# Performance work log

Hardware: AMD Instinct MI355X
Metric: run time of the kernel (lower is better)

The kernel has to match this reference:

```python
import jax, jax.numpy as jnp
import numpy as np

N, E, G = 50000, 800000, 128
IN, HID, HEAD = 1280, 256, 4
DH = HID // HEAD
EPS = 1e-5
ATT_SCALE = 1.0 / np.sqrt(1280.0).astype(np.float32)  # hardcoded in source


def _seg_softmax(x, seg, n):
    # softmax over segments along axis 0; x: [K] or [K, H]
    m = jax.ops.segment_max(x, seg, num_segments=n)
    e = jnp.exp(x - m[seg])
    s = jax.ops.segment_sum(e, seg, num_segments=n)
    return e / s[seg]


def _bn(x, g, b):
    # eval-mode BatchNorm1d with init running stats (mean=0, var=1)
    return g * x * (1.0 / np.sqrt(1.0 + EPS)) + b


def _ln(x, g, b):
    mu = x.mean(-1, keepdims=True)
    var = ((x - mu) ** 2).mean(-1, keepdims=True)
    return g * (x - mu) / jnp.sqrt(var + EPS) + b


def setup_inputs() -> dict:
    key = jax.random.key(0)
    ks = jax.random.split(key, 40)
    rn = lambda i, shp, s=0.05: jax.random.normal(ks[i], shp, jnp.float32) * s
    inp = {
        "h": jax.random.normal(ks[0], (N, IN), jnp.float32),
        "gcn_w0": rn(1, (IN, HID)), "gcn_b0": rn(2, (HID,), 0.01),
        "gcn_w1": rn(3, (HID, HID)), "gcn_b1": rn(4, (HID,), 0.01),
        "bn_gcn0_g": 1.0 + rn(5, (HID,), 0.1), "bn_gcn0_b": rn(6, (HID,), 0.01),
        "bn_gcn1_g": 1.0 + rn(7, (HID,), 0.1), "bn_gcn1_b": rn(8, (HID,), 0.01),
        "gat_w0": rn(9, (IN, HID)), "gat_al0": rn(10, (HEAD, DH)), "gat_ar0": rn(11, (HEAD, DH)), "gat_bias0": rn(12, (HID,), 0.01),
        "gat_w1": rn(13, (HID, HID)), "gat_al1": rn(14, (HEAD, DH)), "gat_ar1": rn(15, (HEAD, DH)), "gat_bias1": rn(16, (HID,), 0.01),
        "bn_gat0_g": 1.0 + rn(17, (HID,), 0.1), "bn_gat0_b": rn(18, (HID,), 0.01),
        "bn_gat1_g": 1.0 + rn(19, (HID,), 0.1), "bn_gat1_b": rn(20, (HID,), 0.01),
        "gate_w": rn(21, (2 * HID, HID)), "gate_b": rn(22, (HID,), 0.01),
        "qw": rn(23, (HEAD, HID, HID)), "kw": rn(24, (HEAD, HID, HID)), "vw": rn(25, (HEAD, HID, HID)),
        "ct_w": rn(26, (HEAD * HID, HID)),
        "ff_w1": rn(27, (HID, 2 * HID)), "ff_b1": rn(28, (2 * HID,), 0.01),
        "ff_w2": rn(29, (2 * HID, HID)), "ff_b2": rn(30, (HID,), 0.01),
        "ln_g": 1.0 + rn(31, (HID,), 0.1), "ln_b": rn(32, (HID,), 0.01),
        "src": jax.random.randint(ks[33], (E,), 0, N, jnp.int32),
        "dst": jax.random.randint(ks[34], (E,), 0, N, jnp.int32),
        "gid": jnp.sort(jax.random.randint(ks[35], (N,), 0, G, jnp.int32)),
        "num_graphs": G,
    }
    return inp


def reference(h, gcn_w0, gcn_b0, gcn_w1, gcn_b1, bn_gcn0_g, bn_gcn0_b, bn_gcn1_g, bn_gcn1_b,
              gat_w0, gat_al0, gat_ar0, gat_bias0, gat_w1, gat_al1, gat_ar1, gat_bias1,
              bn_gat0_g, bn_gat0_b, bn_gat1_g, bn_gat1_b, gate_w, gate_b,
              qw, kw, vw, ct_w, ff_w1, ff_b1, ff_w2, ff_b2, ln_g, ln_b,
              src, dst, gid, num_graphs):
    n = h.shape[0]
    ones_e = jnp.ones(src.shape[0], h.dtype)
    # dgl.mean_nodes per graph
    cnt = jnp.clip(jax.ops.segment_sum(jnp.ones(n, h.dtype), gid, num_segments=num_graphs), 1.0)
    init_avg_h = jax.ops.segment_sum(h, gid, num_segments=num_graphs) / cnt[:, None]
    # GraphConv norm='both', degrees clamped to >=1
    deg_out = jnp.clip(jax.ops.segment_sum(ones_e, src, num_segments=n), 1.0)
    deg_in = jnp.clip(jax.ops.segment_sum(ones_e, dst, num_segments=n), 1.0)
    ns, nd = deg_out ** -0.5, deg_in ** -0.5

    def gcn(x, w, b):
        m = (x * ns[:, None]) @ w  # [N, HID]
        return jax.ops.segment_sum(m[src], dst, num_segments=n) * nd[:, None] + b

    hg = jax.nn.relu(_bn(gcn(h, gcn_w0, gcn_b0), bn_gcn0_g, bn_gcn0_b))
    hg = jax.nn.relu(_bn(gcn(hg, gcn_w1, gcn_b1), bn_gcn1_g, bn_gcn1_b)) + hg

    def gat(x, w, al, ar, b):
        f = (x @ w).reshape(n, HEAD, DH)
        el = (f * al).sum(-1)  # [N, HEAD]
        er = (f * ar).sum(-1)
        e = jax.nn.leaky_relu(el[src] + er[dst], 0.2)  # [E, HEAD]
        alpha = _seg_softmax(e, dst, n)  # edge softmax over incoming edges
        out = jax.ops.segment_sum(alpha[:, :, None] * f[src], dst, num_segments=n)
        return out.reshape(n, HID) + b

    ha = jax.nn.elu(_bn(gat(h, gat_w0, gat_al0, gat_ar0, gat_bias0), bn_gat0_g, bn_gat0_b))
    ha = jax.nn.elu(_bn(gat(ha, gat_w1, gat_al1, gat_ar1, gat_bias1), bn_gat1_g, bn_gat1_b)) + ha

    gate = jax.nn.sigmoid(jnp.concatenate([hg, ha], axis=1) @ gate_w + gate_b)
    x = gate * hg + (1.0 - gate) * ha  # residue_h

    # transformer_block: per-graph node softmax attention
    q = jnp.einsum('nd,hde->nhe', x, qw)
    k = jnp.einsum('nd,hde->nhe', x, kw)
    v = jnp.einsum('nd,hde->nhe', x, vw)
    att = (q * k).sum(-1) * ATT_SCALE  # [N, HEAD]
    alpha = _seg_softmax(att, gid, num_graphs)  # dgl.softmax_nodes per head
    mo = (v * alpha[:, :, None]).reshape(n, HEAD * HID) @ ct_w
    x1 = _ln(mo + x, ln_g, ln_b)
    x2 = _ln(jax.nn.relu(x1 @ ff_w1 + ff_b1) @ ff_w2 + ff_b2 + x1, ln_g, ln_b)

    readout = jax.ops.segment_sum(x2, gid, num_segments=num_graphs)
    return readout, init_avg_h
```

## Files before the change

### kernel.cpp

```cpp
#include <hip/hip_runtime.h>

#define NN 50000
#define NE 800000
#define NG 128
#define DIN 1280
#define HIDDEN 256
#define BNS 0.9999950000374997f
#define ATT_SCALE 0.027950849718747373f
#define LN_EPS 1e-5f

typedef __attribute__((ext_vector_type(8))) short short8;
typedef __attribute__((ext_vector_type(4))) float floatx4;

__device__ __forceinline__ float b2f(unsigned short u) {
  return __uint_as_float(((unsigned int)u) << 16);
}
__device__ __forceinline__ unsigned short f2b(float f) {
  unsigned int x = __float_as_uint(f);
  x += 0x7fffu + ((x >> 16) & 1u);
  return (unsigned short)(x >> 16);
}

__global__ void transpose_w_k(const float* __restrict__ src, unsigned short* __restrict__ dst,
                              int K, int Nc) {
// ... 20 lines not shown
}

__global__ void v_transpose_k(const float* __restrict__ vw, unsigned short* __restrict__ dst) {
  int idx = blockIdx.x * 256 + threadIdx.x;
  if (idx >= 1024 * 256) return;
  int r = idx >> 8;
  int d = idx & 255;
  int hh = r >> 8;
  int e2 = r & 255;
  dst[(size_t)(1024 + r) * 256 + d] = f2b(vw[((size_t)hh * 256 + d) * 256 + e2]);
}

__global__ void cvt_avg_k(const float* __restrict__ h, const int* __restrict__ gid,
                          unsigned short* __restrict__ h_bf, float* __restrict__ out1) {
  int row0 = blockIdx.x * 50;
  int tid = threadIdx.x;
  float acc[5] = {0, 0, 0, 0, 0};
  int cur_g = gid[row0];
  for (int r = 0; r < 50; ++r) {
    int row = row0 + r;
    int g = gid[row];
    if (g != cur_g) {
#pragma unroll
      for (int j = 0; j < 5; ++j) {
        atomicAdd(&out1[(size_t)cur_g * DIN + j * 256 + tid], acc[j]);
        acc[j] = 0.f;
      }
      cur_g = g;
    }
#pragma unroll
    for (int j = 0; j < 5; ++j) {
      float v = h[(size_t)row * DIN + j * 256 + tid];
      acc[j] += v;
      h_bf[(size_t)row * DIN + j * 256 + tid] = f2b(v);
    }
  }
#pragma unroll
  for (int j = 0; j < 5; ++j)
    atomicAdd(&out1[(size_t)cur_g * DIN + j * 256 + tid], acc[j]);
}

__global__ void div_avg_k(const int* __restrict__ start, float* __restrict__ out1) {
  int idx = blockIdx.x * 256 + threadIdx.x;
  if (idx >= NG * DIN) return;
  int g = idx / DIN;
  float cnt = (float)(start[g + 1] - start[g]);
  if (cnt < 1.f) cnt = 1.f;
  out1[idx] /= cnt;
}

__global__ void graph_bounds_k(const int* __restrict__ gid, int* __restrict__ start, int n) {
  int i = blockIdx.x * 256 + threadIdx.x;
  if (i >= n) return;
  int g = gid[i];
  if (i == 0) {
    for (int gg = 0; gg <= g; ++gg) start[gg] = 0;
  } else {
    int gp = gid[i - 1];
    for (int gg = gp + 1; gg <= g; ++gg) start[gg] = i;
  }
  if (i == n - 1) {
    for (int gg = g + 1; gg <= NG; ++gg) start[gg] = n;
  }
}

__global__ void degrees_k(const int* __restrict__ src, const int* __restrict__ dst,
                          int* __restrict__ deg_out, int* __restrict__ deg_in, int e) {
  int i = blockIdx.x * 256 + threadIdx.x;
  if (i >= e) return;
  atomicAdd(&deg_out[src[i]], 1);
  atomicAdd(&deg_in[dst[i]], 1);
}

__global__ void invsqrt_k(const int* __restrict__ deg_out, const int* __restrict__ deg_in,
                          float* __restrict__ ns, float* __restrict__ nd, int n) {
  int i = blockIdx.x * 256 + threadIdx.x;
  if (i >= n) return;
  int a = deg_out[i]; if (a < 1) a = 1;
  int b = deg_in[i];  if (b < 1) b = 1;
  ns[i] = rsqrtf((float)a);
  nd[i] = rsqrtf((float)b);
}

__global__ void scan_k(const int* __restrict__ deg, int* __restrict__ row_ptr, int n) {
  __shared__ int buf[1024];
  __shared__ int carry_s;
  int tid = threadIdx.x;
  if (tid == 0) carry_s = 0;
  __syncthreads();
  for (int base = 0; base < n; base += 1024) {
    int i = base + tid;
    int v = (i < n) ? deg[i] : 0;
    buf[tid] = v;
    __syncthreads();
    for (int off = 1; off < 1024; off <<= 1) {
      int t = (tid >= off) ? buf[tid - off] : 0;
      __syncthreads();
      buf[tid] += t;
      __syncthreads();
    }
    int carry = carry_s;
    if (i < n) row_ptr[i] = carry + buf[tid] - v;
    __syncthreads();
    if (tid == 1023) carry_s = carry + buf[1023];
    __syncthreads();
  }
  if (tid == 0) row_ptr[n] = carry_s;
}

__global__ void fill_csr_k(const int* __restrict__ src, const int* __restrict__ dst,
                           const int* __restrict__ row_ptr, int* __restrict__ fill,
                           int* __restrict__ csr_src, int e) {
  int i = blockIdx.x * 256 + threadIdx.x;
  if (i >= e) return;
  int d = dst[i];
  int pos = row_ptr[d] + atomicAdd(&fill[d], 1);
  csr_src[pos] = src[i];
}

template <int MODE>
__global__ __launch_bounds__(256, 2) void gemm_bf16(const unsigned short* __restrict__ A,
                                                    const unsigned short* __restrict__ Bt,
                                                    void* __restrict__ Cout,
                                                    const float* __restrict__ bias,
                                                    int M, int K, int Nc) {
  __shared__ unsigned short lA[8192];
  __shared__ unsigned short lB[8192];
  const int tid = threadIdx.x;
  const int m0 = blockIdx.x * 128;
  const int n0 = blockIdx.y * 128;
  const int w = tid >> 6;
  const int lane = tid & 63;
  const int wr = (w >> 1) * 64;
  const int wc = (w & 1) * 64;
  const int quad = lane >> 4;
  const int l15 = lane & 15;
  const int js = tid & 7;
  const int mbase = tid >> 3;

  floatx4 acc[4][4];
#pragma unroll
  for (int i = 0; i < 4; ++i)
#pragma unroll
    for (int j = 0; j < 4; ++j) acc[i][j] = (floatx4)0.0f;

  for (int k0 = 0; k0 < K; k0 += 64) {
    __syncthreads();
#pragma unroll
    for (int it = 0; it < 4; ++it) {
      int m = it * 32 + mbase;
      int gm = m0 + m;
      if (gm >= M) gm = M - 1;
      uint4 va = *(const uint4*)(A + (size_t)gm * K + k0 + js * 8);
      int ci_ = js * 128 + (m ^ js);
      *(uint4*)(lA + ci_ * 8) = va;
      int gn = n0 + m;
      uint4 vb = *(const uint4*)(Bt + (size_t)gn * K + k0 + js * 8);
      *(uint4*)(lB + ci_ * 8) = vb;
    }
    __syncthreads();
#pragma unroll
    for (int ks = 0; ks < 2; ++ks) {
      int kb = ks * 4 + quad;
      short8 af[4], bfr[4];
#pragma unroll
      for (int ri = 0; ri < 4; ++ri) {
        int r = wr + ri * 16 + l15;
        af[ri] = *(const short8*)(lA + (kb * 128 + (r ^ kb)) * 8);
      }
#pragma unroll
      for (int ci = 0; ci < 4; ++ci) {
        int c = wc + ci * 16 + l15;
        bfr[ci] = *(const short8*)(lB + (kb * 128 + (c ^ kb)) * 8);
      }
#pragma unroll
      for (int ri = 0; ri < 4; ++ri)
#pragma unroll
        for (int ci = 0; ci < 4; ++ci)
          acc[ri][ci] = __builtin_amdgcn_mfma_f32_16x16x32_bf16(af[ri], bfr[ci], acc[ri][ci], 0, 0, 0);
    }
  }
#pragma unroll
  for (int ri = 0; ri < 4; ++ri) {
    int row = m0 + wr + ri * 16 + quad * 4;
#pragma unroll
    for (int ci = 0; ci < 4; ++ci) {
      int col = n0 + wc + ci * 16 + l15;
      float bv = (MODE == 2) ? bias[col] : 0.f;
#pragma unroll
      for (int r = 0; r < 4; ++r) {
        if (row + r < M) {
          float v = acc[ri][ci][r];
          if (MODE == 2) { v += bv; v = fmaxf(v, 0.f); }
          if (MODE == 1)
            ((float*)Cout)[(size_t)(row + r) * Nc + col] = v;
          else
            ((unsigned short*)Cout)[(size_t)(row + r) * Nc + col] = f2b(v);
        }
      }
    }
  }
}

__global__ void gcn_agg_k(const unsigned short* __restrict__ m, int ldm,
                          const int* __restrict__ row_ptr, const int* __restrict__ csr_src,
                          const float* __restrict__ ns, const float* __restrict__ nd,
                          const float* __restrict__ bias,
                          const float* __restrict__ bng, const float* __restrict__ bnb,
                          const unsigned short* __restrict__ resid, int ldr,
                          unsigned short* __restrict__ out, int ldo) {
  int node = blockIdx.x * 4 + (threadIdx.x >> 6);
  if (node >= NN) return;
  int lane = threadIdx.x & 63;
  int s = row_ptr[node], e = row_ptr[node + 1];
  float a0 = 0, a1 = 0, a2 = 0, a3 = 0;
  for (int i = s; i < e; ++i) {
    int u = csr_src[i];
    float w = ns[u];
    ushort4 v = *(const ushort4*)(m + (size_t)u * ldm + lane * 4);
    a0 += w * b2f(v.x); a1 += w * b2f(v.y); a2 += w * b2f(v.z); a3 += w * b2f(v.w);
  }
  float ndv = nd[node];
  int col = lane * 4;
  float vals[4] = {a0, a1, a2, a3};
  ushort4 o;
#pragma unroll
  for (int c = 0; c < 4; ++c) {
    float v = vals[c] * ndv + bias[col + c];
    v = bng[col + c] * v * BNS + bnb[col + c];
    v = fmaxf(v, 0.f);
    if (resid) v += b2f(resid[(size_t)node * ldr + col + c]);
    ((unsigned short*)&o)[c] = f2b(v);
  }
  *(ushort4*)(out + (size_t)node * ldo + col) = o;
}

__global__ void elr_k(const unsigned short* __restrict__ f, int ldf,
                      const float* __restrict__ al, const float* __restrict__ ar,
                      float* __restrict__ elr) {
  int node = blockIdx.x * 4 + (threadIdx.x >> 6);
  if (node >= NN) return;
  int lane = threadIdx.x & 63;
  int head = lane >> 4;
  int col = lane * 4;
  int dcol = col & 63;
  ushort4 v = *(const ushort4*)(f + (size_t)node * ldf + col);
  float pl = 0, pr = 0;
#pragma unroll
  for (int c = 0; c < 4; ++c) {
    float x = b2f(((unsigned short*)&v)[c]);
    pl += x * al[head * 64 + dcol + c];
    pr += x * ar[head * 64 + dcol + c];
  }
#pragma unroll
  for (int off = 1; off < 16; off <<= 1) {
    pl += __shfl_xor(pl, off);
    pr += __shfl_xor(pr, off);
  }
  if ((lane & 15) == 0) {
    elr[(size_t)node * 8 + head] = pl;
    elr[(size_t)node * 8 + 4 + head] = pr;
  }
}

__global__ void gat_agg_k(const unsigned short* __restrict__ f, int ldf,
                          const int* __restrict__ row_ptr, const int* __restrict__ csr_src,
                          const float* __restrict__ elr,
                          const float* __restrict__ bias,
                          const float* __restrict__ bng, const float* __restrict__ bnb,
                          const unsigned short* __restrict__ resid, int ldr,
                          unsigned short* __restrict__ out, int ldo) {
  int node = blockIdx.x * 4 + (threadIdx.x >> 6);
  if (node >= NN) return;
  int lane = threadIdx.x & 63;
  int s = row_ptr[node], e = row_ptr[node + 1];
  float4 er = *(const float4*)(elr + (size_t)node * 8 + 4);
  float m0 = -1e30f, m1 = -1e30f, m2 = -1e30f, m3 = -1e30f;
  for (int i = s + lane; i < e; i += 64) {
    int u = csr_src[i];
    float4 el = *(const float4*)(elr + (size_t)u * 8);
    float t;
    t = el.x + er.x; t = t > 0.f ? t : 0.2f * t; m0 = fmaxf(m0, t);
    t = el.y + er.y; t = t > 0.f ? t : 0.2f * t; m1 = fmaxf(m1, t);
    t = el.z + er.z; t = t > 0.f ? t : 0.2f * t; m2 = fmaxf(m2, t);
    t = el.w + er.w; t = t > 0.f ? t : 0.2f * t; m3 = fmaxf(m3, t);
  }
#pragma unroll
  for (int off = 1; off < 64; off <<= 1) {
    m0 = fmaxf(m0, __shfl_xor(m0, off));
    m1 = fmaxf(m1, __shfl_xor(m1, off));
    m2 = fmaxf(m2, __shfl_xor(m2, off));
    m3 = fmaxf(m3, __shfl_xor(m3, off));
  }
  float s0 = 0, s1 = 0, s2 = 0, s3 = 0;
  for (int i = s + lane; i < e; i += 64) {
    int u = csr_src[i];
    float4 el = *(const float4*)(elr + (size_t)u * 8);
    float t;
    t = el.x + er.x; t = t > 0.f ? t : 0.2f * t; s0 += expf(t - m0);
    t = el.y + er.y; t = t > 0.f ? t : 0.2f * t; s1 += expf(t - m1);
    t = el.z + er.z; t = t > 0.f ? t : 0.2f * t; s2 += expf(t - m2);
    t = el.w + er.w; t = t > 0.f ? t : 0.2f * t; s3 += expf(t - m3);
  }
#pragma unroll
  for (int off = 1; off < 64; off <<= 1) {
    s0 += __shfl_xor(s0, off);
    s1 += __shfl_xor(s1, off);
    s2 += __shfl_xor(s2, off);
    s3 += __shfl_xor(s3, off);
  }
  int head = lane >> 4;
  float erh = head == 0 ? er.x : head == 1 ? er.y : head == 2 ? er.z : er.w;
  float mh = head == 0 ? m0 : head == 1 ? m1 : head == 2 ? m2 : m3;
  float sh = head == 0 ? s0 : head == 1 ? s1 : head == 2 ? s2 : s3;
  float inv_sh = (sh > 0.f) ? 1.f / sh : 0.f;
  float a0 = 0, a1 = 0, a2 = 0, a3 = 0;
  for (int i = s; i < e; ++i) {
    int u = csr_src[i];
    float t = elr[(size_t)u * 8 + head] + erh;
    t = t > 0.f ? t : 0.2f * t;
    float wgt = expf(t - mh) * inv_sh;
    ushort4 v = *(const ushort4*)(f + (size_t)u * ldf + lane * 4);
    a0 += wgt * b2f(v.x); a1 += wgt * b2f(v.y); a2 += wgt * b2f(v.z); a3 += wgt * b2f(v.w);
  }
  int col = lane * 4;
  float vals[4] = {a0, a1, a2, a3};
  ushort4 o;
#pragma unroll
  for (int c = 0; c < 4; ++c) {
    float v = vals[c] + bias[col + c];
    v = bng[col + c] * v * BNS + bnb[col + c];
    v = (v > 0.f) ? v : (expf(v) - 1.f);
    if (resid) v += b2f(resid[(size_t)node * ldr + col + c]);
    ((unsigned short*)&o)[c] = f2b(v);
  }
  *(ushort4*)(out + (size_t)node * ldo + col) = o;
}

__global__ void combine_k(const float* __restrict__ glogit, const float* __restrict__ gate_b,
                          const unsigned short* __restrict__ xcat,
                          float* __restrict__ xf, unsigned short* __restrict__ xb) {
  int idx = blockIdx.x * 256 + threadIdx.x;
  if (idx >= NN * 64) return;
  int node = idx >> 6;
  int c = (idx & 63) * 4;
  float4 gl = *(const float4*)(glogit + (size_t)node * HIDDEN + c);
  ushort4 hgv = *(const ushort4*)(xcat + (size_t)node * 512 + c);
  ushort4 hav = *(const ushort4*)(xcat + (size_t)node * 512 + 256 + c);
  float4 o;
  float g;
  g = 1.f / (1.f + expf(-(gl.x + gate_b[c + 0]))); o.x = g * b2f(hgv.x) + (1.f - g) * b2f(hav.x);
  g = 1.f / (1.f + expf(-(gl.y + gate_b[c + 1]))); o.y = g * b2f(hgv.y) + (1.f - g) * b2f(hav.y);
  g = 1.f / (1.f + expf(-(gl.z + gate_b[c + 2]))); o.z = g * b2f(hgv.z) + (1.f - g) * b2f(hav.z);
  g = 1.f / (1.f + expf(-(gl.w + gate_b[c + 3]))); o.w = g * b2f(hgv.w) + (1.f - g) * b2f(hav.w);
  *(float4*)(xf + (size_t)node * HIDDEN + c) = o;
  ushort4 ob;
  ob.x = f2b(o.x); ob.y = f2b(o.y); ob.z = f2b(o.z); ob.w = f2b(o.w);
  *(ushort4*)(xb + (size_t)node * HIDDEN + c) = ob;
}

__global__ void att2_k(const unsigned short* __restrict__ yv, const unsigned short* __restrict__ xb,
                       float* __restrict__ att) {
  int node = blockIdx.x * 4 + (threadIdx.x >> 6);
  if (node >= NN) return;
  int lane = threadIdx.x & 63;
  const unsigned short* y = yv + (size_t)node * 2048;
  ushort4 xv = *(const ushort4*)(xb + (size_t)node * 256 + lane * 4);
  float x0 = b2f(xv.x), x1 = b2f(xv.y), x2 = b2f(xv.z), x3 = b2f(xv.w);
#pragma unroll
  for (int h = 0; h < 4; ++h) {
    ushort4 yv4 = *(const ushort4*)(y + h * 256 + lane * 4);
    float p = b2f(yv4.x) * x0 + b2f(yv4.y) * x1 + b2f(yv4.z) * x2 + b2f(yv4.w) * x3;
#pragma unroll
    for (int off = 1; off < 64; off <<= 1) p += __shfl_xor(p, off);
    if (lane == 0) att[(size_t)node * 4 + h] = p * ATT_SCALE;
  }
}

__global__ void gsoftmax_k(const float* __restrict__ att, const int* __restrict__ start,
                           float* __restrict__ alpha) {
  int g = blockIdx.x;
  int s = start[g], e = start[g + 1];
  int tid = threadIdx.x;
  __shared__ float red[256];
  __shared__ float mh[4], sh[4];
  float lm[4] = {-1e30f, -1e30f, -1e30f, -1e30f};
  for (int i = s + tid; i < e; i += 256) {
    float4 a = *(const float4*)(att + (size_t)i * 4);
    lm[0] = fmaxf(lm[0], a.x); lm[1] = fmaxf(lm[1], a.y);
    lm[2] = fmaxf(lm[2], a.z); lm[3] = fmaxf(lm[3], a.w);
  }
#pragma unroll
  for (int h = 0; h < 4; ++h) {
    red[tid] = lm[h]; __syncthreads();
    for (int off = 128; off > 0; off >>= 1) {
      if (tid < off) red[tid] = fmaxf(red[tid], red[tid + off]);
      __syncthreads();
    }
    if (tid == 0) mh[h] = red[0];
    __syncthreads();
  }
  float ls[4] = {0, 0, 0, 0};
  for (int i = s + tid; i < e; i += 256) {
    float4 a = *(const float4*)(att + (size_t)i * 4);
    ls[0] += expf(a.x - mh[0]); ls[1] += expf(a.y - mh[1]);
    ls[2] += expf(a.z - mh[2]); ls[3] += expf(a.w - mh[3]);
  }
#pragma unroll
  for (int h = 0; h < 4; ++h) {
    red[tid] = ls[h]; __syncthreads();
    for (int off = 128; off > 0; off >>= 1) {
      if (tid < off) red[tid] += red[tid + off];
      __syncthreads();
    }
    if (tid == 0) sh[h] = red[0];
    __syncthreads();
  }
  for (int i = s + tid; i < e; i += 256) {
    float4 a = *(const float4*)(att + (size_t)i * 4);
    float4 o;
    o.x = expf(a.x - mh[0]) / sh[0];
    o.y = expf(a.y - mh[1]) / sh[1];
    o.z = expf(a.z - mh[2]) / sh[2];
    o.w = expf(a.w - mh[3]) / sh[3];
    *(float4*)(alpha + (size_t)i * 4) = o;
  }
}

__global__ void scalev_k(const unsigned short* __restrict__ yv, const float* __restrict__ alpha,
                         unsigned short* __restrict__ vs) {
  int idx = blockIdx.x * 256 + threadIdx.x;
  if (idx >= NN * 256) return;
  int node = idx >> 8;
  int c = (idx & 255) * 4;
  int h = c >> 8;
  float a = alpha[(size_t)node * 4 + h];
  ushort4 v = *(const ushort4*)(yv + (size_t)node * 2048 + 1024 + c);
  ushort4 o;
  o.x = f2b(b2f(v.x) * a); o.y = f2b(b2f(v.y) * a);
  o.z = f2b(b2f(v.z) * a); o.w = f2b(b2f(v.w) * a);
  *(ushort4*)(vs + (size_t)node * 1024 + c) = o;
}

__global__ void ln1_k(const float* __restrict__ mo, const float* __restrict__ x,
                      const float* __restrict__ g, const float* __restrict__ b,
                      float* __restrict__ x1f, unsigned short* __restrict__ x1b) {
  int node = blockIdx.x * 4 + (threadIdx.x >> 6);
  if (node >= NN) return;
  int lane = threadIdx.x & 63;
  int c = lane * 4;
  float4 a = *(const float4*)(mo + (size_t)node * HIDDEN + c);
  float4 xx = *(const float4*)(x + (size_t)node * HIDDEN + c);
  float v0 = a.x + xx.x, v1 = a.y + xx.y, v2 = a.z + xx.z, v3 = a.w + xx.w;
  float sm = v0 + v1 + v2 + v3;
#pragma unroll
  for (int off = 1; off < 64; off <<= 1) sm += __shfl_xor(sm, off);
  float mu = sm * (1.f / 256.f);
  float d0 = v0 - mu, d1 = v1 - mu, d2 = v2 - mu, d3 = v3 - mu;
  float sq = d0 * d0 + d1 * d1 + d2 * d2 + d3 * d3;
#pragma unroll
  for (int off = 1; off < 64; off <<= 1) sq += __shfl_xor(sq, off);
  float inv = rsqrtf(sq * (1.f / 256.f) + LN_EPS);
  float4 o;
  o.x = g[c + 0] * d0 * inv + b[c + 0];
  o.y = g[c + 1] * d1 * inv + b[c + 1];
  o.z = g[c + 2] * d2 * inv + b[c + 2];
  o.w = g[c + 3] * d3 * inv + b[c + 3];
  *(float4*)(x1f + (size_t)node * HIDDEN + c) = o;
  ushort4 ob;
  ob.x = f2b(o.x); ob.y = f2b(o.y); ob.z = f2b(o.z); ob.w = f2b(o.w);
  *(ushort4*)(x1b + (size_t)node * HIDDEN + c) = ob;
}

__global__ void ln2_k(const float* __restrict__ ff2o, const float* __restrict__ ffb2,
                      const float* __restrict__ x1f,
                      const float* __restrict__ g, const float* __restrict__ b,
                      float* __restrict__ x2) {
  int node = blockIdx.x * 4 + (threadIdx.x >> 6);
  if (node >= NN) return;
  int lane = threadIdx.x & 63;
  int c = lane * 4;
  float4 a = *(const float4*)(ff2o + (size_t)node * HIDDEN + c);
  float4 xx = *(const float4*)(x1f + (size_t)node * HIDDEN + c);
  float v0 = a.x + ffb2[c + 0] + xx.x, v1 = a.y + ffb2[c + 1] + xx.y;
  float v2 = a.z + ffb2[c + 2] + xx.z, v3 = a.w + ffb2[c + 3] + xx.w;
  float sm = v0 + v1 + v2 + v3;
#pragma unroll
  for (int off = 1; off < 64; off <<= 1) sm += __shfl_xor(sm, off);
  float mu = sm * (1.f / 256.f);
  float d0 = v0 - mu, d1 = v1 - mu, d2 = v2 - mu, d3 = v3 - mu;
  float sq = d0 * d0 + d1 * d1 + d2 * d2 + d3 * d3;
#pragma unroll
  for (int off = 1; off < 64; off <<= 1) sq += __shfl_xor(sq, off);
  float inv = rsqrtf(sq * (1.f / 256.f) + LN_EPS);
  float4 o;
  o.x = g[c + 0] * d0 * inv + b[c + 0];
  o.y = g[c + 1] * d1 * inv + b[c + 1];
  o.z = g[c + 2] * d2 * inv + b[c + 2];
  o.w = g[c + 3] * d3 * inv + b[c + 3];
  *(float4*)(x2 + (size_t)node * HIDDEN + c) = o;
}

__global__ void readout_k(const float* __restrict__ x2, const int* __restrict__ start,
                          float* __restrict__ out0) {
  int g = blockIdx.x;
  int c = threadIdx.x;
  float acc = 0.f;
  for (int i = start[g]; i < start[g + 1]; ++i) acc += x2[(size_t)i * HIDDEN + c];
  out0[(size_t)g * HIDDEN + c] = acc;
}

static const size_t OFF_BUFA   = 0;
static const size_t OFF_XCAT   = 307200000;
static const size_t OFF_GLOGIT = OFF_XCAT + 51200000;
static const size_t OFF_XF     = OFF_GLOGIT + 51200000;
static const size_t OFF_XB     = OFF_XF + 51200000;
static const size_t OFF_VS     = OFF_XB + 25600000;
static const size_t OFF_ATT    = OFF_VS + 102400000;
static const size_t OFF_ALPHA  = OFF_ATT + 800000;
static const size_t OFF_ELR0   = OFF_ALPHA + 800000;
static const size_t OFF_ELR1   = OFF_ELR0 + 1600000;
static const size_t OFF_START  = OFF_ELR1 + 1600000;
static const size_t OFF_DEGO   = OFF_START + 1024;
static const size_t OFF_DEGI   = OFF_DEGO + 200704;
static const size_t OFF_NS     = OFF_DEGI + 200704;
static const size_t OFF_ND     = OFF_NS + 200704;
static const size_t OFF_ROWP   = OFF_ND + 200704;
static const size_t OFF_FILL   = OFF_ROWP + 200704;
static const size_t OFF_CSRS   = OFF_FILL + 200704;
static const size_t OFF_W01T   = OFF_CSRS + 3200000;
static const size_t OFF_W1T    = OFF_W01T + 1310720;
static const size_t OFF_W1GT   = OFF_W1T + 131072;
static const size_t OFF_GATEWT = OFF_W1GT + 131072;
static const size_t OFF_WMVT   = OFF_GATEWT + 262144;
static const size_t OFF_CTWT   = OFF_WMVT + 1572864;
static const size_t OFF_FFW1T  = OFF_CTWT + 524288;
static const size_t OFF_FFW2T  = OFF_FFW1T + 262144;
static const size_t WS_NEED    = OFF_FFW2T + 262144;

extern "C" void kernel_launch(void* const* d_in, const int* in_sizes, int n_in,
                              void* d_out, int out_size, void* d_ws, size_t ws_size,
                              hipStream_t stream) {
  if (ws_size < WS_NEED) return;

  const float* h       = (const float*)d_in[0];
  const float* gcn_w0  = (const float*)d_in[1];
  const float* gcn_b0  = (const float*)d_in[2];
  const float* gcn_w1  = (const float*)d_in[3];
  const float* gcn_b1  = (const float*)d_in[4];
  const float* bn_gcn0_g = (const float*)d_in[5];
  const float* bn_gcn0_b = (const float*)d_in[6];
  const float* bn_gcn1_g = (const float*)d_in[7];
  const float* bn_gcn1_b = (const float*)d_in[8];
  const float* gat_w0  = (const float*)d_in[9];
  const float* gat_al0 = (const float*)d_in[10];
  const float* gat_ar0 = (const float*)d_in[11];
  const float* gat_bias0 = (const float*)d_in[12];
  const float* gat_w1  = (const float*)d_in[13];
  const float* gat_al1 = (const float*)d_in[14];
  const float* gat_ar1 = (const float*)d_in[15];
  const float* gat_bias1 = (const float*)d_in[16];
  const float* bn_gat0_g = (const float*)d_in[17];
  const float* bn_gat0_b = (const float*)d_in[18];
  const float* bn_gat1_g = (const float*)d_in[19];
  const float* bn_gat1_b = (const float*)d_in[20];
  const float* gate_w  = (const float*)d_in[21];
  const float* gate_b  = (const float*)d_in[22];
  const float* qw      = (const float*)d_in[23];
  const float* kw      = (const float*)d_in[24];
  const float* vw      = (const float*)d_in[25];
  const float* ct_w    = (const float*)d_in[26];
  const float* ff_w1   = (const float*)d_in[27];
  const float* ff_b1   = (const float*)d_in[28];
  const float* ff_w2   = (const float*)d_in[29];
  const float* ff_b2   = (const float*)d_in[30];
  const float* ln_g    = (const float*)d_in[31];
  const float* ln_b    = (const float*)d_in[32];
  const int* srcv = (const int*)d_in[33];
  const int* dstv = (const int*)d_in[34];
  const int* gid  = (const int*)d_in[35];

  char* ws = (char*)d_ws;
  unsigned short* h_bf = (unsigned short*)(ws + OFF_BUFA);
  unsigned short* c01  = (unsigned short*)(ws + OFF_BUFA + 128000000);
  unsigned short* hg0  = (unsigned short*)(ws + OFF_BUFA + 179200000);
  unsigned short* ha0  = (unsigned short*)(ws + OFF_BUFA + 204800000);
  unsigned short* m1   = (unsigned short*)(ws + OFF_BUFA + 230400000);
  unsigned short* f1   = (unsigned short*)(ws + OFF_BUFA + 256000000);
  unsigned short* yv   = (unsigned short*)(ws + OFF_BUFA);
  unsigned short* ff1o = (unsigned short*)(ws + OFF_BUFA);
  float* ff2o          = (float*)(ws + OFF_BUFA + 51200000);
  float* x2            = (float*)(ws + OFF_BUFA + 102400000);
  unsigned short* xcat = (unsigned short*)(ws + OFF_XCAT);
  float* glogit        = (float*)(ws + OFF_GLOGIT);
  float* mo            = (float*)(ws + OFF_GLOGIT);
  float* xf            = (float*)(ws + OFF_XF);
  unsigned short* xb   = (unsigned short*)(ws + OFF_XB);
  unsigned short* vs   = (unsigned short*)(ws + OFF_VS);
  float* x1f           = (float*)(ws + OFF_VS);
  unsigned short* x1b  = (unsigned short*)(ws + OFF_VS + 51200000);
  float* att           = (float*)(ws + OFF_ATT);
  float* alpha         = (float*)(ws + OFF_ALPHA);
  float* elr0          = (float*)(ws + OFF_ELR0);
  float* elr1          = (float*)(ws + OFF_ELR1);
  int* start   = (int*)(ws + OFF_START);
  int* deg_out = (int*)(ws + OFF_DEGO);
  int* deg_in  = (int*)(ws + OFF_DEGI);
  float* ns    = (float*)(ws + OFF_NS);
  float* nd    = (float*)(ws + OFF_ND);
  int* row_ptr = (int*)(ws + OFF_ROWP);
  int* fill    = (int*)(ws + OFF_FILL);
  int* csr_src = (int*)(ws + OFF_CSRS);
  unsigned short* w01t   = (unsigned short*)(ws + OFF_W01T);
  unsigned short* w1t    = (unsigned short*)(ws + OFF_W1T);
  unsigned short* w1gt   = (unsigned short*)(ws + OFF_W1GT);
  unsigned short* gatewt = (unsigned short*)(ws + OFF_GATEWT);
  unsigned short* wmvt   = (unsigned short*)(ws + OFF_WMVT);
  unsigned short* ctwt   = (unsigned short*)(ws + OFF_CTWT);
  unsigned short* ffw1t  = (unsigned short*)(ws + OFF_FFW1T);
  unsigned short* ffw2t  = (unsigned short*)(ws + OFF_FFW2T);

  float* out0 = (float*)d_out;
  float* out1 = out0 + NG * HIDDEN;

  hipMemsetAsync(deg_out, 0, NN * 4, stream);
  hipMemsetAsync(deg_in, 0, NN * 4, stream);
  hipMemsetAsync(fill, 0, NN * 4, stream);
  hipMemsetAsync(out1, 0, NG * DIN * 4, stream);

  transpose_w_k<<<(1280 * 256 + 255) / 256, 256, 0, stream>>>(gcn_w0, w01t, 1280, 256);
  transpose_w_k<<<(1280 * 256 + 255) / 256, 256, 0, stream>>>(gat_w0, w01t + 256 * 1280, 1280, 256);
  transpose_w_k<<<(256 * 256 + 255) / 256, 256, 0, stream>>>(gcn_w1, w1t, 256, 256);
  transpose_w_k<<<(256 * 256 + 255) / 256, 256, 0, stream>>>(gat_w1, w1gt, 256, 256);
  transpose_w_k<<<(512 * 256 + 255) / 256, 256, 0, stream>>>(gate_w, gatewt, 512, 256);
  mw_k<<<1024, 256, 0, stream>>>(qw, kw, wmvt);
  v_transpose_k<<<1024, 256, 0, stream>>>(vw, wmvt);
  transpose_w_k<<<(1024 * 256 + 255) / 256, 256, 0, stream>>>(ct_w, ctwt, 1024, 256);
  transpose_w_k<<<(256 * 512 + 255) / 256, 256, 0, stream>>>(ff_w1, ffw1t, 256, 512);
  transpose_w_k<<<(512 * 256 + 255) / 256, 256, 0, stream>>>(ff_w2, ffw2t, 512, 256);

  graph_bounds_k<<<(NN + 255) / 256, 256, 0, stream>>>(gid, start, NN);
  degrees_k<<<(NE + 255) / 256, 256, 0, stream>>>(srcv, dstv, deg_out, deg_in, NE);
  invsqrt_k<<<(NN + 255) / 256, 256, 0, stream>>>(deg_out, deg_in, ns, nd, NN);
  scan_k<<<1, 1024, 0, stream>>>(deg_in, row_ptr, NN);
  fill_csr_k<<<(NE + 255) / 256, 256, 0, stream>>>(srcv, dstv, row_ptr, fill, csr_src, NE);

  cvt_avg_k<<<NN / 50, 256, 0, stream>>>(h, gid, h_bf, out1);
  div_avg_k<<<(NG * DIN + 255) / 256, 256, 0, stream>>>(start, out1);

  const int MB = (NN + 127) / 128;
  gemm_bf16<0><<<dim3(MB, 4), 256, 0, stream>>>(h_bf, w01t, c01, nullptr, NN, 1280, 512);
  gcn_agg_k<<<NN / 4, 256, 0, stream>>>(c01, 512, row_ptr, csr_src, ns, nd,
                                        gcn_b0, bn_gcn0_g, bn_gcn0_b, nullptr, 0, hg0, 256);
  elr_k<<<NN / 4, 256, 0, stream>>>(c01 + 256, 512, gat_al0, gat_ar0, elr0);
  gat_agg_k<<<NN / 4, 256, 0, stream>>>(c01 + 256, 512, row_ptr, csr_src, elr0,
                                        gat_bias0, bn_gat0_g, bn_gat0_b, nullptr, 0, ha0, 256);
  gemm_bf16<0><<<dim3(MB, 2), 256, 0, stream>>>(hg0, w1t, m1, nullptr, NN, 256, 256);
  gcn_agg_k<<<NN / 4, 256, 0, stream>>>(m1, 256, row_ptr, csr_src, ns, nd,
                                        gcn_b1, bn_gcn1_g, bn_gcn1_b, hg0, 256, xcat, 512);
  gemm_bf16<0><<<dim3(MB, 2), 256, 0, stream>>>(ha0, w1gt, f1, nullptr, NN, 256, 256);
  elr_k<<<NN / 4, 256, 0, stream>>>(f1, 256, gat_al1, gat_ar1, elr1);
  gat_agg_k<<<NN / 4, 256, 0, stream>>>(f1, 256, row_ptr, csr_src, elr1,
                                        gat_bias1, bn_gat1_g, bn_gat1_b, ha0, 256, xcat + 256, 512);
  gemm_bf16<1><<<dim3(MB, 2), 256, 0, stream>>>(xcat, gatewt, glogit, nullptr, NN, 512, 256);
  combine_k<<<NN / 4, 256, 0, stream>>>(glogit, gate_b, xcat, xf, xb);
  gemm_bf16<0><<<dim3(MB, 16), 256, 0, stream>>>(xb, wmvt, yv, nullptr, NN, 256, 2048);
  att2_k<<<NN / 4, 256, 0, stream>>>(yv, xb, att);
  gsoftmax_k<<<NG, 256, 0, stream>>>(att, start, alpha);
  scalev_k<<<NN, 256, 0, stream>>>(yv, alpha, vs);
  gemm_bf16<1><<<dim3(MB, 2), 256, 0, stream>>>(vs, ctwt, mo, nullptr, NN, 1024, 256);
  ln1_k<<<NN / 4, 256, 0, stream>>>(mo, xf, ln_g, ln_b, x1f, x1b);
  gemm_bf16<2><<<dim3(MB, 4), 256, 0, stream>>>(x1b, ffw1t, ff1o, ff_b1, NN, 256, 512);
  gemm_bf16<1><<<dim3(MB, 2), 256, 0, stream>>>(ff1o, ffw2t, ff2o, nullptr, NN, 512, 256);
  ln2_k<<<NN / 4, 256, 0, stream>>>(ff2o, ff_b2, x1f, ln_g, ln_b, x2);
  readout_k<<<NG, 256, 0, stream>>>(x2, start, out0);
}
```

Before: 1.864 ms.

## Fuse attention score and V-scaling into GEMMs, parallelize scan, bf16 intermediates

Replaces the single-block serial prefix scan with a three-kernel block scan. The QK-score dot product moves into the Q/K GEMM epilogue using atomics, and the V half is written to a compact buffer. Alpha scaling of V is folded into the A-load of the context GEMM, which removes the att2 and scalev kernels. Grid axes are swapped so column tiles of the same row block run adjacently for better A reuse in cache. Intermediate activations (gate logits, mo, x1, ff2o, x2) are stored in bf16 instead of fp32 to cut memory traffic, at some cost in accuracy.

```diff
diff --git a/kernel.cpp b/kernel.cpp
--- a/kernel.cpp
+++ b/kernel.cpp
@@ -126,30 +126,45 @@
   nd[i] = rsqrtf((float)b);
 }
 
-__global__ void scan_k(const int* __restrict__ deg, int* __restrict__ row_ptr, int n) {
-  __shared__ int buf[1024];
-  __shared__ int carry_s;
-  int tid = threadIdx.x;
-  if (tid == 0) carry_s = 0;
+__global__ void scan_local_k(const int* __restrict__ deg, int* __restrict__ row_ptr,
+                             int* __restrict__ bsum) {
+  __shared__ int buf[256];
+  int b = blockIdx.x, t = threadIdx.x;
+  int i = b * 256 + t;
+  int v = (i < NN) ? deg[i] : 0;
+  buf[t] = v;
   __syncthreads();
-  for (int base = 0; base < n; base += 1024) {
-    int i = base + tid;
-    int v = (i < n) ? deg[i] : 0;
-    buf[tid] = v;
-    __syncthreads();
-    for (int off = 1; off < 1024; off <<= 1) {
-      int t = (tid >= off) ? buf[tid - off] : 0;
-      __syncthreads();
-      buf[tid] += t;
-      __syncthreads();
-    }
-    int carry = carry_s;
-    if (i < n) row_ptr[i] = carry + buf[tid] - v;
-    __syncthreads();
-    if (tid == 1023) carry_s = carry + buf[1023];
-    __syncthreads();
-  }
-  if (tid == 0) row_ptr[n] = carry_s;
+  for (int off = 1; off < 256; off <<= 1) {
+    int tv = (t >= off) ? buf[t - off] : 0;
+    __syncthreads();
+    buf[t] += tv;
+    __syncthreads();
+  }
+  if (i < NN) row_ptr[i] = buf[t] - v;
+  if (t == 255) bsum[b] = buf[255];
+}
+
+__global__ void scan_bsum_k(int* __restrict__ bsum, int* __restrict__ boff, int nb,
+                            int* __restrict__ row_ptr) {
+  __shared__ int buf[256];
+  int t = threadIdx.x;
+  int v = (t < nb) ? bsum[t] : 0;
+  buf[t] = v;
+  __syncthreads();
+  for (int off = 1; off < 256; off <<= 1) {
+    int tv = (t >= off) ? buf[t - off] : 0;
+    __syncthreads();
+    buf[t] += tv;
+    __syncthreads();
+  }
+  if (t < nb) boff[t] = buf[t] - v;
+  if (t == 0) row_ptr[NN] = NE;
+}
+
+__global__ void scan_add_k(int* __restrict__ row_ptr, const int* __restrict__ boff) {
+  int i = blockIdx.x * 256 + threadIdx.x;
+  if (i >= NN) return;
+  row_ptr[i] += boff[blockIdx.x];
 }
 
 __global__ void fill_csr_k(const int* __restrict__ src, const int* __restrict__ dst,
@@ -167,12 +182,16 @@
                                                     const unsigned short* __restrict__ Bt,
                                                     void* __restrict__ Cout,
                                                     const float* __restrict__ bias,
-                                                    int M, int K, int Nc) {
-  __shared__ unsigned short lA[8192];
-  __shared__ unsigned short lB[8192];
+                                                    int M, int K, int Nc,
+                                                    const unsigned short* __restrict__ xtile,
+                                                    float* __restrict__ attp,
+                                                    const float* __restrict__ ascale) {
+  __shared__ unsigned short sbuf[16384];
+  unsigned short* lA = sbuf;
+  unsigned short* lB = sbuf + 8192;
   const int tid = threadIdx.x;
-  const int m0 = blockIdx.x * 128;
-  const int n0 = blockIdx.y * 128;
+  const int n0 = blockIdx.x * 128;
+  const int m0 = blockIdx.y * 128;
   const int w = tid >> 6;
   const int lane = tid & 63;
   const int wr = (w >> 1) * 64;
@@ -196,6 +215,12 @@
       int gm = m0 + m;
       if (gm >= M) gm = M - 1;
       uint4 va = *(const uint4*)(A + (size_t)gm * K + k0 + js * 8);
+      if (MODE == 5) {
+        float s = ascale[(size_t)gm * 4 + (k0 >> 8)];
+        unsigned short* pp = (unsigned short*)&va;
+#pragma unroll
+        for (int c = 0; c < 8; ++c) pp[c] = f2b(b2f(pp[c]) * s);
+      }
       int ci_ = js * 128 + (m ^ js);
       *(uint4*)(lA + ci_ * 8) = va;
       int gn = n0 + m;
@@ -224,6 +249,43 @@
           acc[ri][ci] = __builtin_amdgcn_mfma_f32_16x16x32_bf16(af[ri], bfr[ci], acc[ri][ci], 0, 0, 0);
     }
   }
+
+  if (MODE == 4 && n0 < 1024) {
+    __syncthreads();
+    int cb = n0 & 255;
+#pragma unroll
+    for (int it2 = 0; it2 < 8; ++it2) {
+      int linear = it2 * 256 + tid;
+      int rr = linear >> 4;
+      int c8 = (linear & 15) * 8;
+      int gr = m0 + rr;
+      if (gr >= M) gr = M - 1;
+      *(uint4*)(sbuf + rr * 128 + c8) = *(const uint4*)(xtile + (size_t)gr * 256 + cb + c8);
+    }
+    __syncthreads();
+    int head = n0 >> 8;
+#pragma unroll
+    for (int ri = 0; ri < 4; ++ri) {
+      int lrow = wr + ri * 16 + quad * 4;
+#pragma unroll
+      for (int r = 0; r < 4; ++r) {
+        float p = 0.f;
+#pragma unroll
+        for (int ci = 0; ci < 4; ++ci)
+          p += acc[ri][ci][r] * b2f(sbuf[(lrow + r) * 128 + wc + ci * 16 + l15]);
+        p += __shfl_xor(p, 1);
+        p += __shfl_xor(p, 2);
+        p += __shfl_xor(p, 4);
+        p += __shfl_xor(p, 8);
+        if (l15 == 0) {
+          int grow = m0 + lrow + r;
+          if (grow < M) atomicAdd(&attp[(size_t)grow * 4 + head], p * ATT_SCALE);
+        }
+      }
+    }
+    return;
+  }
+
 #pragma unroll
   for (int ri = 0; ri < 4; ++ri) {
     int row = m0 + wr + ri * 16 + quad * 4;
@@ -238,6 +300,8 @@
           if (MODE == 2) { v += bv; v = fmaxf(v, 0.f); }
           if (MODE == 1)
             ((float*)Cout)[(size_t)(row + r) * Nc + col] = v;
+          else if (MODE == 4)
+            ((unsigned short*)Cout)[(size_t)(row + r) * 1024 + col - 1024] = f2b(v);
           else
             ((unsigned short*)Cout)[(size_t)(row + r) * Nc + col] = f2b(v);
         }
@@ -381,44 +445,23 @@
   *(ushort4*)(out + (size_t)node * ldo + col) = o;
 }
 
-__global__ void combine_k(const float* __restrict__ glogit, const float* __restrict__ gate_b,
+__global__ void combine_k(const unsigned short* __restrict__ glogit, const float* __restrict__ gate_b,
                           const unsigned short* __restrict__ xcat,
-                          float* __restrict__ xf, unsigned short* __restrict__ xb) {
+                          unsigned short* __restrict__ xb) {
   int idx = blockIdx.x * 256 + threadIdx.x;
   if (idx >= NN * 64) return;
   int node = idx >> 6;
   int c = (idx & 63) * 4;
-  float4 gl = *(const float4*)(glogit + (size_t)node * HIDDEN + c);
+  ushort4 gl = *(const ushort4*)(glogit + (size_t)node * HIDDEN + c);
   ushort4 hgv = *(const ushort4*)(xcat + (size_t)node * 512 + c);
   ushort4 hav = *(const ushort4*)(xcat + (size_t)node * 512 + 256 + c);
-  float4 o;
+  ushort4 ob;
   float g;
-  g = 1.f / (1.f + expf(-(gl.x + gate_b[c + 0]))); o.x = g * b2f(hgv.x) + (1.f - g) * b2f(hav.x);
-  g = 1.f / (1.f + expf(-(gl.y + gate_b[c + 1]))); o.y = g * b2f(hgv.y) + (1.f - g) * b2f(hav.y);
-  g = 1.f / (1.f + expf(-(gl.z + gate_b[c + 2]))); o.z = g * b2f(hgv.z) + (1.f - g) * b2f(hav.z);
-  g = 1.f / (1.f + expf(-(gl.w + gate_b[c + 3]))); o.w = g * b2f(hgv.w) + (1.f - g) * b2f(hav.w);
-  *(float4*)(xf + (size_t)node * HIDDEN + c) = o;
-  ushort4 ob;
-  ob.x = f2b(o.x); ob.y = f2b(o.y); ob.z = f2b(o.z); ob.w = f2b(o.w);
+  g = 1.f / (1.f + expf(-(b2f(gl.x) + gate_b[c + 0]))); ob.x = f2b(g * b2f(hgv.x) + (1.f - g) * b2f(hav.x));
+  g = 1.f / (1.f + expf(-(b2f(gl.y) + gate_b[c + 1]))); ob.y = f2b(g * b2f(hgv.y) + (1.f - g) * b2f(hav.y));
+  g = 1.f / (1.f + expf(-(b2f(gl.z) + gate_b[c + 2]))); ob.z = f2b(g * b2f(hgv.z) + (1.f - g) * b2f(hav.z));
+  g = 1.f / (1.f + expf(-(b2f(gl.w) + gate_b[c + 3]))); ob.w = f2b(g * b2f(hgv.w) + (1.f - g) * b2f(hav.w));
   *(ushort4*)(xb + (size_t)node * HIDDEN + c) = ob;
-}
-
-__global__ void att2_k(const unsigned short* __restrict__ yv, const unsigned short* __restrict__ xb,
-                       float* __restrict__ att) {
-  int node = blockIdx.x * 4 + (threadIdx.x >> 6);
-  if (node >= NN) return;
-  int lane = threadIdx.x & 63;
-  const unsigned short* y = yv + (size_t)node * 2048;
-  ushort4 xv = *(const ushort4*)(xb + (size_t)node * 256 + lane * 4);
-  float x0 = b2f(xv.x), x1 = b2f(xv.y), x2 = b2f(xv.z), x3 = b2f(xv.w);
-#pragma unroll
-  for (int h = 0; h < 4; ++h) {
-    ushort4 yv4 = *(const ushort4*)(y + h * 256 + lane * 4);
-    float p = b2f(yv4.x) * x0 + b2f(yv4.y) * x1 + b2f(yv4.z) * x2 + b2f(yv4.w) * x3;
-#pragma unroll
-    for (int off = 1; off < 64; off <<= 1) p += __shfl_xor(p, off);
-    if (lane == 0) att[(size_t)node * 4 + h] = p * ATT_SCALE;
-  }
 }
 
 __global__ void gsoftmax_k(const float* __restrict__ att, const int* __restrict__ start,
@@ -471,31 +514,17 @@
   }
 }
 
-__global__ void scalev_k(const unsigned short* __restrict__ yv, const float* __restrict__ alpha,
-                         unsigned short* __restrict__ vs) {
-  int idx = blockIdx.x * 256 + threadIdx.x;
-  if (idx >= NN * 256) return;
-  int node = idx >> 8;
-  int c = (idx & 255) * 4;
-  int h = c >> 8;
-  float a = alpha[(size_t)node * 4 + h];
-  ushort4 v = *(const ushort4*)(yv + (size_t)node * 2048 + 1024 + c);
-  ushort4 o;
-  o.x = f2b(b2f(v.x) * a); o.y = f2b(b2f(v.y) * a);
-  o.z = f2b(b2f(v.z) * a); o.w = f2b(b2f(v.w) * a);
-  *(ushort4*)(vs + (size_t)node * 1024 + c) = o;
-}
-
-__global__ void ln1_k(const float* __restrict__ mo, const float* __restrict__ x,
+__global__ void ln1_k(const unsigned short* __restrict__ mo, const unsigned short* __restrict__ x,
                       const float* __restrict__ g, const float* __restrict__ b,
-                      float* __restrict__ x1f, unsigned short* __restrict__ x1b) {
+                      unsigned short* __restrict__ x1) {
   int node = blockIdx.x * 4 + (threadIdx.x >> 6);
   if (node >= NN) return;
   int lane = threadIdx.x & 63;
   int c = lane * 4;
-  float4 a = *(const float4*)(mo + (size_t)node * HIDDEN + c);
-  float4 xx = *(const float4*)(x + (size_t)node * HIDDEN + c);
-  float v0 = a.x + xx.x, v1 = a.y + xx.y, v2 = a.z + xx.z, v3 = a.w + xx.w;
+  ushort4 a = *(const ushort4*)(mo + (size_t)node * HIDDEN + c);
+  ushort4 xx = *(const ushort4*)(x + (size_t)node * HIDDEN + c);
+  float v0 = b2f(a.x) + b2f(xx.x), v1 = b2f(a.y) + b2f(xx.y);
+  float v2 = b2f(a.z) + b2f(xx.z), v3 = b2f(a.w) + b2f(xx.w);
   float sm = v0 + v1 + v2 + v3;
 #pragma unroll
   for (int off = 1; off < 64; off <<= 1) sm += __shfl_xor(sm, off);
@@ -505,29 +534,26 @@
 #pragma unroll
   for (int off = 1; off < 64; off <<= 1) sq += __shfl_xor(sq, off);
   float inv = rsqrtf(sq * (1.f / 256.f) + LN_EPS);
-  float4 o;
-  o.x = g[c + 0] * d0 * inv + b[c + 0];
-  o.y = g[c + 1] * d1 * inv + b[c + 1];
-  o.z = g[c + 2] * d2 * inv + b[c + 2];
-  o.w = g[c + 3] * d3 * inv + b[c + 3];
-  *(float4*)(x1f + (size_t)node * HIDDEN + c) = o;
   ushort4 ob;
-  ob.x = f2b(o.x); ob.y = f2b(o.y); ob.z = f2b(o.z); ob.w = f2b(o.w);
-  *(ushort4*)(x1b + (size_t)node * HIDDEN + c) = ob;
-}
-
-__global__ void ln2_k(const float* __restrict__ ff2o, const float* __restrict__ ffb2,
-                      const float* __restrict__ x1f,
+  ob.x = f2b(g[c + 0] * d0 * inv + b[c + 0]);
+  ob.y = f2b(g[c + 1] * d1 * inv + b[c + 1]);
+  ob.z = f2b(g[c + 2] * d2 * inv + b[c + 2]);
+  ob.w = f2b(g[c + 3] * d3 * inv + b[c + 3]);
+  *(ushort4*)(x1 + (size_t)node * HIDDEN + c) = ob;
+}
+
+__global__ void ln2_k(const unsigned short* __restrict__ ff2o, const float* __restrict__ ffb2,
+                      const unsigned short* __restrict__ x1,
                       const float* __restrict__ g, const float* __restrict__ b,
-                      float* __restrict__ x2) {
+                      unsigned short* __restrict__ x2) {
   int node = blockIdx.x * 4 + (threadIdx.x >> 6);
   if (node >= NN) return;
   int lane = threadIdx.x & 63;
   int c = lane * 4;
-  float4 a = *(const float4*)(ff2o + (size_t)node * HIDDEN + c);
-  float4 xx = *(const float4*)(x1f + (size_t)node * HIDDEN + c);
-  float v0 = a.x + ffb2[c + 0] + xx.x, v1 = a.y + ffb2[c + 1] + xx.y;
-  float v2 = a.z + ffb2[c + 2] + xx.z, v3 = a.w + ffb2[c + 3] + xx.w;
+  ushort4 a = *(const ushort4*)(ff2o + (size_t)node * HIDDEN + c);
+  ushort4 xx = *(const ushort4*)(x1 + (size_t)node * HIDDEN + c);
+  float v0 = b2f(a.x) + ffb2[c + 0] + b2f(xx.x), v1 = b2f(a.y) + ffb2[c + 1] + b2f(xx.y);
+  float v2 = b2f(a.z) + ffb2[c + 2] + b2f(xx.z), v3 = b2f(a.w) + ffb2[c + 3] + b2f(xx.w);
   float sm = v0 + v1 + v2 + v3;
 #pragma unroll
   for (int off = 1; off < 64; off <<= 1) sm += __shfl_xor(sm, off);
@@ -537,30 +563,35 @@
 #pragma unroll
   for (int off = 1; off < 64; off <<= 1) sq += __shfl_xor(sq, off);
   float inv = rsqrtf(sq * (1.f / 256.f) + LN_EPS);
-  float4 o;
-  o.x = g[c + 0] * d0 * inv + b[c + 0];
-  o.y = g[c + 1] * d1 * inv + b[c + 1];
-  o.z = g[c + 2] * d2 * inv + b[c + 2];
-  o.w = g[c + 3] * d3 * inv + b[c + 3];
-  *(float4*)(x2 + (size_t)node * HIDDEN + c) = o;
-}
-
-__global__ void readout_k(const float* __restrict__ x2, const int* __restrict__ start,
+  ushort4 ob;
+  ob.x = f2b(g[c + 0] * d0 * inv + b[c + 0]);
+  ob.y = f2b(g[c + 1] * d1 * inv + b[c + 1]);
+  ob.z = f2b(g[c + 2] * d2 * inv + b[c + 2]);
+  ob.w = f2b(g[c + 3] * d3 * inv + b[c + 3]);
+  *(ushort4*)(x2 + (size_t)node * HIDDEN + c) = ob;
+}
+
+__global__ void readout_k(const unsigned short* __restrict__ x2, const int* __restrict__ start,
                           float* __restrict__ out0) {
   int g = blockIdx.x;
   int c = threadIdx.x;
   float acc = 0.f;
-  for (int i = start[g]; i < start[g + 1]; ++i) acc += x2[(size_t)i * HIDDEN + c];
+  for (int i = start[g]; i < start[g + 1]; ++i) acc += b2f(x2[(size_t)i * HIDDEN + c]);
   out0[(size_t)g * HIDDEN + c] = acc;
 }
 
 static const size_t OFF_BUFA   = 0;
-static const size_t OFF_XCAT   = 307200000;
-static const size_t OFF_GLOGIT = OFF_XCAT + 51200000;
-static const size_t OFF_XF     = OFF_GLOGIT + 51200000;
-static const size_t OFF_XB     = OFF_XF + 51200000;
-static const size_t OFF_VS     = OFF_XB + 25600000;
-static const size_t OFF_ATT    = OFF_VS + 102400000;
+static const size_t OFF_C01    = 128000000;
+static const size_t OFF_HG0    = 179200000;
+static const size_t OFF_HA0    = 204800000;
+static const size_t OFF_M1     = 230400000;
+static const size_t OFF_F1     = 256000000;
+static const size_t OFF_XCAT   = 281600000;
+static const size_t OFF_GLOGIT = 332800000;
+static const size_t OFF_XB     = 358400000;
+static const size_t OFF_MO     = 384000000;
+static const size_t OFF_X1     = 409600000;
+static const size_t OFF_ATT    = 435200000;
 static const size_t OFF_ALPHA  = OFF_ATT + 800000;
 static const size_t OFF_ELR0   = OFF_ALPHA + 800000;
 static const size_t OFF_ELR1   = OFF_ELR0 + 1600000;
@@ -571,13 +602,15 @@
 static const size_t OFF_ND     = OFF_NS + 200704;
 static const size_t OFF_ROWP   = OFF_ND + 200704;
 static const size_t OFF_FILL   = OFF_ROWP + 200704;
-static const size_t OFF_CSRS   = OFF_FILL + 200704;
+static const size_t OFF_BSUM   = OFF_FILL + 200704;
+static const size_t OFF_BOFF   = OFF_BSUM + 1024;
+static const size_t OFF_CSRS   = OFF_BOFF + 1024;
 static const size_t OFF_W01T   = OFF_CSRS + 3200000;
 static const size_t OFF_W1T    = OFF_W01T + 1310720;
 static const size_t OFF_W1GT   = OFF_W1T + 131072;
 static const size_t OFF_GATEWT = OFF_W1GT + 131072;
 static const size_t OFF_WMVT   = OFF_GATEWT + 262144;
-static const size_t OFF_CTWT   = OFF_WMVT + 1572864;
+static const size_t OFF_CTWT   = OFF_WMVT + 1048576;
 static const size_t OFF_FFW1T  = OFF_CTWT + 524288;
 static const size_t OFF_FFW2T  = OFF_FFW1T + 262144;
 static const size_t WS_NEED    = OFF_FFW2T + 262144;
@@ -626,23 +659,20 @@
 
   char* ws = (char*)d_ws;
   unsigned short* h_bf = (unsigned short*)(ws + OFF_BUFA);
-  unsigned short* c01  = (unsigned short*)(ws + OFF_BUFA + 128000000);
-  unsigned short* hg0  = (unsigned short*)(ws + OFF_BUFA + 179200000);
-  unsigned short* ha0  = (unsigned short*)(ws + OFF_BUFA + 204800000);
-  unsigned short* m1   = (unsigned short*)(ws + OFF_BUFA + 230400000);
-  unsigned short* f1   = (unsigned short*)(ws + OFF_BUFA + 256000000);
   unsigned short* yv   = (unsigned short*)(ws + OFF_BUFA);
   unsigned short* ff1o = (unsigned short*)(ws + OFF_BUFA);
-  float* ff2o          = (float*)(ws + OFF_BUFA + 51200000);
-  float* x2            = (float*)(ws + OFF_BUFA + 102400000);
+  unsigned short* ff2o = (unsigned short*)(ws + OFF_BUFA + 51200000);
+  unsigned short* x2   = (unsigned short*)(ws + OFF_BUFA + 76800000);
+  unsigned short* c01  = (unsigned short*)(ws + OFF_C01);
+  unsigned short* hg0  = (unsigned short*)(ws + OFF_HG0);
+  unsigned short* ha0  = (unsigned short*)(ws + OFF_HA0);
+  unsigned short* m1   = (unsigned short*)(ws + OFF_M1);
+  unsigned short* f1   = (unsigned short*)(ws + OFF_F1);
   unsigned short* xcat = (unsigned short*)(ws + OFF_XCAT);
-  float* glogit        = (float*)(ws + OFF_GLOGIT);
-  float* mo            = (float*)(ws + OFF_GLOGIT);
-  float* xf            = (float*)(ws + OFF_XF);
+  unsigned short* glogit = (unsigned short*)(ws + OFF_GLOGIT);
   unsigned short* xb   = (unsigned short*)(ws + OFF_XB);
-  unsigned short* vs   = (unsigned short*)(ws + OFF_VS);
-  float* x1f           = (float*)(ws + OFF_VS);
-  unsigned short* x1b  = (unsigned short*)(ws + OFF_VS + 51200000);
+  unsigned short* mo   = (unsigned short*)(ws + OFF_MO);
+  unsigned short* x1   = (unsigned short*)(ws + OFF_X1);
   float* att           = (float*)(ws + OFF_ATT);
   float* alpha         = (float*)(ws + OFF_ALPHA);
   float* elr0          = (float*)(ws + OFF_ELR0);
@@ -654,6 +684,8 @@
   float* nd    = (float*)(ws + OFF_ND);
   int* row_ptr = (int*)(ws + OFF_ROWP);
   int* fill    = (int*)(ws + OFF_FILL);
+  int* bsum    = (int*)(ws + OFF_BSUM);
+  int* boff    = (int*)(ws + OFF_BOFF);
   int* csr_src = (int*)(ws + OFF_CSRS);
   unsigned short* w01t   = (unsigned short*)(ws + OFF_W01T);
   unsigned short* w1t    = (unsigned short*)(ws + OFF_W1T);
@@ -671,6 +703,7 @@
   hipMemsetAsync(deg_in, 0, NN * 4, stream);
   hipMemsetAsync(fill, 0, NN * 4, stream);
   hipMemsetAsync(out1, 0, NG * DIN * 4, stream);
+  hipMemsetAsync(att, 0, NN * 4 * 4, stream);
 
   transpose_w_k<<<(1280 * 256 + 255) / 256, 256, 0, stream>>>(gcn_w0, w01t, 1280, 256);
   transpose_w_k<<<(1280 * 256 + 255) / 256, 256, 0, stream>>>(gat_w0, w01t + 256 * 1280, 1280, 256);
@@ -686,36 +719,45 @@
   graph_bounds_k<<<(NN + 255) / 256, 256, 0, stream>>>(gid, start, NN);
   degrees_k<<<(NE + 255) / 256, 256, 0, stream>>>(srcv, dstv, deg_out, deg_in, NE);
   invsqrt_k<<<(NN + 255) / 256, 256, 0, stream>>>(deg_out, deg_in, ns, nd, NN);
-  scan_k<<<1, 1024, 0, stream>>>(deg_in, row_ptr, NN);
+  const int NB_SCAN = (NN + 255) / 256;
+  scan_local_k<<<NB_SCAN, 256, 0, stream>>>(deg_in, row_ptr, bsum);
+  scan_bsum_k<<<1, 256, 0, stream>>>(bsum, boff, NB_SCAN, row_ptr);
+  scan_add_k<<<NB_SCAN, 256, 0, stream>>>(row_ptr, boff);
   fill_csr_k<<<(NE + 255) / 256, 256, 0, stream>>>(srcv, dstv, row_ptr, fill, csr_src, NE);
 
   cvt_avg_k<<<NN / 50, 256, 0, stream>>>(h, gid, h_bf, out1);
   div_avg_k<<<(NG * DIN + 255) / 256, 256, 0, stream>>>(start, out1);
 
   const int MB = (NN + 127) / 128;
-  gemm_bf16<0><<<dim3(MB, 4), 256, 0, stream>>>(h_bf, w01t, c01, nullptr, NN, 1280, 512);
+  gemm_bf16<0><<<dim3(4, MB), 256, 0, stream>>>(h_bf, w01t, c01, nullptr, NN, 1280, 512,
+                                                nullptr, nullptr, nullptr);
   gcn_agg_k<<<NN / 4, 256, 0, stream>>>(c01, 512, row_ptr, csr_src, ns, nd,
                                         gcn_b0, bn_gcn0_g, bn_gcn0_b, nullptr, 0, hg0, 256);
   elr_k<<<NN / 4, 256, 0, stream>>>(c01 + 256, 512, gat_al0, gat_ar0, elr0);
   gat_agg_k<<<NN / 4, 256, 0, stream>>>(c01 + 256, 512, row_ptr, csr_src, elr0,
                                         gat_bias0, bn_gat0_g, bn_gat0_b, nullptr, 0, ha0, 256);
-  gemm_bf16<0><<<dim3(MB, 2), 256, 0, stream>>>(hg0, w1t, m1, nullptr, NN, 256, 256);
+  gemm_bf16<0><<<dim3(2, MB), 256, 0, stream>>>(hg0, w1t, m1, nullptr, NN, 256, 256,
+                                                nullptr, nullptr, nullptr);
   gcn_agg_k<<<NN / 4, 256, 0, stream>>>(m1, 256, row_ptr, csr_src, ns, nd,
                                         gcn_b1, bn_gcn1_g, bn_gcn1_b, hg0, 256, xcat, 512);
-  gemm_bf16<0><<<dim3(MB, 2), 256, 0, stream>>>(ha0, w1gt, f1, nullptr, NN, 256, 256);
+  gemm_bf16<0><<<dim3(2, MB), 256, 0, stream>>>(ha0, w1gt, f1, nullptr, NN, 256, 256,
+                                                nullptr, nullptr, nullptr);
   elr_k<<<NN / 4, 256, 0, stream>>>(f1, 256, gat_al1, gat_ar1, elr1);
   gat_agg_k<<<NN / 4, 256, 0, stream>>>(f1, 256, row_ptr, csr_src, elr1,
                                         gat_bias1, bn_gat1_g, bn_gat1_b, ha0, 256, xcat + 256, 512);
-  gemm_bf16<1><<<dim3(MB, 2), 256, 0, stream>>>(xcat, gatewt, glogit, nullptr, NN, 512, 256);
-  combine_k<<<NN / 4, 256, 0, stream>>>(glogit, gate_b, xcat, xf, xb);
-  gemm_bf16<0><<<dim3(MB, 16), 256, 0, stream>>>(xb, wmvt, yv, nullptr, NN, 256, 2048);
-  att2_k<<<NN / 4, 256, 0, stream>>>(yv, xb, att);
+  gemm_bf16<0><<<dim3(2, MB), 256, 0, stream>>>(xcat, gatewt, glogit, nullptr, NN, 512, 256,
+                                                nullptr, nullptr, nullptr);
+  combine_k<<<NN / 4, 256, 0, stream>>>(glogit, gate_b, xcat, xb);
+  gemm_bf16<4><<<dim3(16, MB), 256, 0, stream>>>(xb, wmvt, yv, nullptr, NN, 256, 2048,
+                                                 xb, att, nullptr);
   gsoftmax_k<<<NG, 256, 0, stream>>>(att, start, alpha);
-  scalev_k<<<NN, 256, 0, stream>>>(yv, alpha, vs);
-  gemm_bf16<1><<<dim3(MB, 2), 256, 0, stream>>>(vs, ctwt, mo, nullptr, NN, 1024, 256);
-  ln1_k<<<NN / 4, 256, 0, stream>>>(mo, xf, ln_g, ln_b, x1f, x1b);
-  gemm_bf16<2><<<dim3(MB, 4), 256, 0, stream>>>(x1b, ffw1t, ff1o, ff_b1, NN, 256, 512);
-  gemm_bf16<1><<<dim3(MB, 2), 256, 0, stream>>>(ff1o, ffw2t, ff2o, nullptr, NN, 512, 256);
-  ln2_k<<<NN / 4, 256, 0, stream>>>(ff2o, ff_b2, x1f, ln_g, ln_b, x2);
+  gemm_bf16<5><<<dim3(2, MB), 256, 0, stream>>>(yv, ctwt, mo, nullptr, NN, 1024, 256,
+                                                nullptr, nullptr, alpha);
+  ln1_k<<<NN / 4, 256, 0, stream>>>(mo, xb, ln_g, ln_b, x1);
+  gemm_bf16<2><<<dim3(4, MB), 256, 0, stream>>>(x1, ffw1t, ff1o, ff_b1, NN, 256, 512,
+                                                nullptr, nullptr, nullptr);
+  gemm_bf16<0><<<dim3(2, MB), 256, 0, stream>>>(ff1o, ffw2t, ff2o, nullptr, NN, 512, 256,
+                                                nullptr, nullptr, nullptr);
+  ln2_k<<<NN / 4, 256, 0, stream>>>(ff2o, ff_b2, x1, ln_g, ln_b, x2);
   readout_k<<<NG, 256, 0, stream>>>(x2, start, out0);
 }
```

New measurement: 1.750 ms. 6.1% less time.
